# Optimization experiments

Hardware: AMD Instinct MI355X
Metric: run time of the kernel (lower is better)

## Reference

```python
import jax, jax.numpy as jnp
import numpy as np

EPS = 1e-5

def _bn(x, g, b):
    # BatchNorm1d in training mode: stats over (batch, length) dims, biased var
    mean = jnp.mean(x, axis=(0, 2), keepdims=True)
    var = jnp.var(x, axis=(0, 2), keepdims=True)
    return (x - mean) * jax.lax.rsqrt(var + EPS) * g[None, :, None] + b[None, :, None]

def _conv1x1(x, w, b):
    # pointwise Conv1d: [B,C,T] x [O,C] -> [B,O,T]
    return jnp.einsum('bct,oc->bot', x, w) + b[None, :, None]

def setup_inputs() -> dict:
    key = jax.random.key(0)
    ks = jax.random.split(key, 4)
    B, C, T = 32, 1024, 2048
    x = jax.random.normal(ks[0], (B, C, T), dtype=jnp.float32)
    w1 = jax.random.normal(ks[1], (256, 1024), dtype=jnp.float32) * (1.0 / np.sqrt(1024))
    w2 = jax.random.normal(ks[2], (64, 256), dtype=jnp.float32) * (1.0 / np.sqrt(256))
    return {
        'x': x,
        'bn1_g': jnp.ones((1024,), jnp.float32), 'bn1_b': jnp.zeros((1024,), jnp.float32),
        'w1': w1, 'b1': jnp.zeros((256,), jnp.float32),
        'bn2_g': jnp.ones((256,), jnp.float32), 'bn2_b': jnp.zeros((256,), jnp.float32),
        'w2': w2, 'b2': jnp.zeros((64,), jnp.float32),
    }

def reference(x, bn1_g, bn1_b, w1, b1, bn2_g, bn2_b, w2, b2):
    # reduction layer: BN -> 1x1 conv -> ReLU (1024 -> 256)
    h = jax.nn.relu(_conv1x1(_bn(x, bn1_g, bn1_b), w1, b1))
    # out layer: BN -> 1x1 conv, no activation (256 -> 64)
    out = _conv1x1(_bn(h, bn2_g, bn2_b), w2, b2)
    o = out.shape[1]
    mu = out[:, : o // 2, :]
    logvar = out[:, o // 2 :, :]
    return (mu, logvar)
```

## Files before the change

### kernel.cpp

```cpp
#include <hip/hip_runtime.h>

#define B_  32
#define C1  1024
#define C2  256
#define T_  2048
#define EPSF 1e-5f
#define CPAD 72

typedef __attribute__((ext_vector_type(8))) short bf16x8;
typedef __attribute__((ext_vector_type(4))) float f32x4;

static __device__ __forceinline__ unsigned short f2bf(float f) {
    union { float f; unsigned u; } v; v.f = f;
    unsigned r = v.u + 0x7fffu + ((v.u >> 16) & 1u);
    return (unsigned short)(r >> 16);
}
static __device__ __forceinline__ void g2l16(const void* g, void* l) {
    __builtin_amdgcn_global_load_lds(
        (const __attribute__((address_space(1))) unsigned int*)g,
        (__attribute__((address_space(3))) unsigned int*)l, 16, 0, 0);
}

__global__ __launch_bounds__(256) void k_prep(const float* __restrict__ x,
        unsigned short* __restrict__ xT, float* __restrict__ psum, float* __restrict__ psq) {
    __shared__ unsigned short tile[64 * CPAD];
    __shared__ float red[256];
    int ct = blockIdx.x, b = blockIdx.y, tid = threadIdx.x;
    int c0 = ct * 64;
    int cl = tid >> 2, t4 = tid & 3;
    const float* xrow = x + (size_t)b * C1 * T_ + (size_t)(c0 + cl) * T_;
    float s = 0.f, sq = 0.f;
    for (int t0 = 0; t0 < T_; t0 += 64) {
        #pragma unroll
        for (int j = 0; j < 4; ++j) {
            int tl = j * 16 + t4 * 4;
            float4 v = *(const float4*)(xrow + t0 + tl);
            s  += v.x + v.y + v.z + v.w;
            sq += v.x * v.x + v.y * v.y + v.z * v.z + v.w * v.w;
            tile[(tl + 0) * CPAD + cl] = f2bf(v.x);
            tile[(tl + 1) * CPAD + cl] = f2bf(v.y);
            tile[(tl + 2) * CPAD + cl] = f2bf(v.z);
            tile[(tl + 3) * CPAD + cl] = f2bf(v.w);
        }
        __syncthreads();
        #pragma unroll
        for (int j = 0; j < 2; ++j) {
            int w = tid + j * 256;
            int tl = w >> 3, cu = w & 7;
            uint4 vv = *(const uint4*)&tile[tl * CPAD + cu * 8];
            *(uint4*)&xT[((size_t)b * T_ + t0 + tl) * C1 + c0 + cu * 8] = vv;
        }
        __syncthreads();
    }
    red[tid] = s; __syncthreads();
    if (tid < 64)
        psum[(size_t)b * C1 + c0 + tid] = red[4*tid] + red[4*tid+1] + red[4*tid+2] + red[4*tid+3];
    __syncthreads();
    red[tid] = sq; __syncthreads();
    if (tid < 64)
        psq[(size_t)b * C1 + c0 + tid]  = red[4*tid] + red[4*tid+1] + red[4*tid+2] + red[4*tid+3];
}

__global__ __launch_bounds__(256) void k_fold1(const float* __restrict__ w1,
        const float* __restrict__ b1, const float* __restrict__ g1, const float* __restrict__ bb1,
        const float* __restrict__ psum, const float* __restrict__ psq,
        unsigned short* __restrict__ w1e, float* __restrict__ b1e) {
    int o = blockIdx.x, tid = threadIdx.x;
    int c = tid * 4;
    float4 s = {0,0,0,0}, sq = {0,0,0,0};
    for (int b = 0; b < B_; ++b) {
        float4 a = *(const float4*)(psum + (size_t)b * C1 + c);
        float4 q = *(const float4*)(psq  + (size_t)b * C1 + c);
        s.x += a.x; s.y += a.y; s.z += a.z; s.w += a.w;
        sq.x += q.x; sq.y += q.y; sq.z += q.z; sq.w += q.w;
    }
    const float n = (float)(B_ * T_);
    float4 gg = *(const float4*)(g1 + c);
    float4 bv = *(const float4*)(bb1 + c);
    float m0 = s.x / n, m1 = s.y / n, m2 = s.z / n, m3 = s.w / n;
    float sc0 = gg.x * rsqrtf(sq.x / n - m0 * m0 + EPSF);
    float sc1 = gg.y * rsqrtf(sq.y / n - m1 * m1 + EPSF);
    float sc2 = gg.z * rsqrtf(sq.z / n - m2 * m2 + EPSF);
    float sc3 = gg.w * rsqrtf(sq.w / n - m3 * m3 + EPSF);
    float sh0 = bv.x - m0 * sc0, sh1 = bv.y - m1 * sc1;
    float sh2 = bv.z - m2 * sc2, sh3 = bv.w - m3 * sc3;
    float4 w = ((const float4*)(w1 + (size_t)o * C1))[tid];
    float p = w.x * sh0 + w.y * sh1 + w.z * sh2 + w.w * sh3;
    uint2 pk;
    pk.x = (unsigned)f2bf(w.x * sc0) | ((unsigned)f2bf(w.y * sc1) << 16);
    pk.y = (unsigned)f2bf(w.z * sc2) | ((unsigned)f2bf(w.w * sc3) << 16);
    *((uint2*)(w1e + (size_t)o * C1 + c)) = pk;
    __shared__ float rs[256];
    rs[tid] = p; __syncthreads();
    for (int off = 128; off > 0; off >>= 1) {
        if (tid < off) rs[tid] += rs[tid + off];
        __syncthreads();
    }
    if (tid == 0) b1e[o] = b1[o] + rs[0];
}

__global__ __launch_bounds__(256, 2) void k_gemm1(const unsigned short* __restrict__ xT,
        const unsigned short* __restrict__ w1e, const float* __restrict__ b1e,
        unsigned short* __restrict__ hT, float* __restrict__ p2s, float* __restrict__ p2q) {
    __shared__ unsigned short sA[256 * 32];
    __shared__ unsigned short sB[128 * 32];
    int bn = blockIdx.x, b = blockIdx.y;
    int tid = threadIdx.x;
    int wave = tid >> 6, lane = tid & 63;
    int wm = wave >> 1, wn = wave & 1;
    int l15 = lane & 15, q = lane >> 4;
    f32x4 acc[8][4] = {};
    const unsigned short* xblk = xT + ((size_t)b * T_ + (size_t)bn * 128) * C1;

    for (int k0 = 0; k0 < C1; k0 += 32) {
        #pragma unroll
        for (int i = 0; i < 4; ++i) {
            int idx = (wave * 4 + i) * 64 + lane;
            int row = idx >> 2, cq = idx & 3;
            g2l16(w1e + (size_t)row * C1 + k0 + cq * 8, &sA[(wave * 4 + i) * 512]);
        }
        #pragma unroll
        for (int i = 0; i < 2; ++i) {
            int idx = (wave * 2 + i) * 64 + lane;
            int row = idx >> 2, cq = idx & 3;
            g2l16(xblk + (size_t)row * C1 + k0 + cq * 8, &sB[(wave * 2 + i) * 512]);
        }
        __syncthreads();
        bf16x8 bfr[4];
        #pragma unroll
        for (int ni = 0; ni < 4; ++ni)
            bfr[ni] = *((const bf16x8*)&sB[(wn * 64 + ni * 16 + l15) * 32 + q * 8]);
        #pragma unroll
        for (int mi = 0; mi < 8; ++mi) {
            bf16x8 af = *((const bf16x8*)&sA[(wm * 128 + mi * 16 + l15) * 32 + q * 8]);
            #pragma unroll
            for (int ni = 0; ni < 4; ++ni)
                acc[mi][ni] = __builtin_amdgcn_mfma_f32_16x16x32_bf16(af, bfr[ni], acc[mi][ni], 0, 0, 0);
        }
        __syncthreads();
    }
    int obase = wm * 128;
    int tbase = bn * 128 + wn * 64;
    int prow = (b * 16 + bn) * 2 + wn;
    #pragma unroll
    for (int mi = 0; mi < 8; ++mi) {
        int og = obase + mi * 16 + q * 4;
        float4 bias = *(const float4*)&b1e[og];
        float s0 = 0, s1 = 0, s2 = 0, s3 = 0, q0 = 0, q1 = 0, q2 = 0, q3 = 0;
        #pragma unroll
        for (int ni = 0; ni < 4; ++ni) {
            int t = tbase + ni * 16 + l15;
            float v0 = fmaxf(acc[mi][ni][0] + bias.x, 0.f);
            float v1 = fmaxf(acc[mi][ni][1] + bias.y, 0.f);
            float v2 = fmaxf(acc[mi][ni][2] + bias.z, 0.f);
            float v3 = fmaxf(acc[mi][ni][3] + bias.w, 0.f);
            s0 += v0; q0 += v0 * v0;  s1 += v1; q1 += v1 * v1;
            s2 += v2; q2 += v2 * v2;  s3 += v3; q3 += v3 * v3;
            uint2 pk;
            pk.x = (unsigned)f2bf(v0) | ((unsigned)f2bf(v1) << 16);
            pk.y = (unsigned)f2bf(v2) | ((unsigned)f2bf(v3) << 16);
            *(uint2*)&hT[((size_t)b * T_ + t) * C2 + og] = pk;
        }
        #pragma unroll
        for (int m = 1; m <= 8; m <<= 1) {
            s0 += __shfl_xor(s0, m); s1 += __shfl_xor(s1, m);
            s2 += __shfl_xor(s2, m); s3 += __shfl_xor(s3, m);
            q0 += __shfl_xor(q0, m); q1 += __shfl_xor(q1, m);
            q2 += __shfl_xor(q2, m); q3 += __shfl_xor(q3, m);
        }
        if (l15 == 0) {
            *(float4*)&p2s[(size_t)prow * C2 + og] = make_float4(s0, s1, s2, s3);
            *(float4*)&p2q[(size_t)prow * C2 + og] = make_float4(q0, q1, q2, q3);
        }
    }
}

__global__ __launch_bounds__(256) void k_fold2(const float* __restrict__ w2,
        const float* __restrict__ b2, const float* __restrict__ g2, const float* __restrict__ bb2,
        const float* __restrict__ p2s, const float* __restrict__ p2q,
        unsigned short* __restrict__ w2e, float* __restrict__ b2e) {
    int o = blockIdx.x, tid = threadIdx.x;
    float s = 0.f, sq = 0.f;
    for (int r = 0; r < 1024; ++r) {
        s  += p2s[(size_t)r * C2 + tid];
        sq += p2q[(size_t)r * C2 + tid];
    }
    const float n = (float)(B_ * T_);
    float mean = s / n;
    float sc = g2[tid] * rsqrtf(sq / n - mean * mean + EPSF);
    float sh = bb2[tid] - mean * sc;
    float w = w2[(size_t)o * C2 + tid];
    float p = w * sh;
    w2e[(size_t)o * C2 + tid] = f2bf(w * sc);
    __shared__ float rs[256];
    rs[tid] = p; __syncthreads();
    for (int off = 128; off > 0; off >>= 1) {
        if (tid < off) rs[tid] += rs[tid + off];
        __syncthreads();
    }
    if (tid == 0) b2e[o] = b2[o] + rs[0];
}

__global__ __launch_bounds__(256) void k_gemm2(const unsigned short* __restrict__ hT,
        const unsigned short* __restrict__ w2e, const float* __restrict__ b2e,
        float* __restrict__ out) {
    __shared__ unsigned short sA[64 * 32];
    __shared__ unsigned short sB[128 * 32];
    int bn = blockIdx.x, b = blockIdx.y;
    int tid = threadIdx.x;
    int wave = tid >> 6, lane = tid & 63;
    int l15 = lane & 15, q = lane >> 4;
    f32x4 acc[4][2] = {};
    const unsigned short* hblk = hT + ((size_t)b * T_ + (size_t)bn * 128) * C2;

    for (int k0 = 0; k0 < C2; k0 += 32) {
        {
            int idx = wave * 64 + lane;
            int row = idx >> 2, cq = idx & 3;
            g2l16(w2e + (size_t)row * C2 + k0 + cq * 8, &sA[wave * 512]);
        }
        #pragma unroll
        for (int i = 0; i < 2; ++i) {
            int idx = (wave * 2 + i) * 64 + lane;
            int row = idx >> 2, cq = idx & 3;
            g2l16(hblk + (size_t)row * C2 + k0 + cq * 8, &sB[(wave * 2 + i) * 512]);
        }
        __syncthreads();
        bf16x8 af[4], bfr[2];
        #pragma unroll
        for (int mi = 0; mi < 4; ++mi)
            af[mi] = *((const bf16x8*)&sA[(mi * 16 + l15) * 32 + q * 8]);
        #pragma unroll
        for (int ni = 0; ni < 2; ++ni)
            bfr[ni] = *((const bf16x8*)&sB[(wave * 32 + ni * 16 + l15) * 32 + q * 8]);
        #pragma unroll
        for (int mi = 0; mi < 4; ++mi)
            #pragma unroll
            for (int ni = 0; ni < 2; ++ni)
                acc[mi][ni] = __builtin_amdgcn_mfma_f32_16x16x32_bf16(af[mi], bfr[ni], acc[mi][ni], 0, 0, 0);
        __syncthreads();
    }
    int tbase = bn * 128 + wave * 32;
    #pragma unroll
    for (int mi = 0; mi < 4; ++mi) {
        #pragma unroll
        for (int reg = 0; reg < 4; ++reg) {
            int o = mi * 16 + q * 4 + reg;
            float bias = b2e[o];
            size_t base = (o < 32)
                ? ((size_t)b * 32 * T_ + (size_t)o * T_)
                : (2097152u + (size_t)b * 32 * T_ + (size_t)(o - 32) * T_);
            #pragma unroll
            for (int ni = 0; ni < 2; ++ni) {
                int t = tbase + ni * 16 + l15;
                out[base + t] = acc[mi][ni][reg] + bias;
            }
        }
    }
}

extern "C" void kernel_launch(void* const* d_in, const int* in_sizes, int n_in,
                              void* d_out, int out_size, void* d_ws, size_t ws_size,
                              hipStream_t stream) {
    const float* x   = (const float*)d_in[0];
    const float* g1  = (const float*)d_in[1];
    const float* bb1 = (const float*)d_in[2];
    const float* w1  = (const float*)d_in[3];
    const float* b1  = (const float*)d_in[4];
    const float* g2  = (const float*)d_in[5];
    const float* bb2 = (const float*)d_in[6];
    const float* w2  = (const float*)d_in[7];
    const float* b2  = (const float*)d_in[8];
    float* out = (float*)d_out;

    char* ws = (char*)d_ws;
    float* b1e  = (float*)(ws + 0);
    float* b2e  = (float*)(ws + 4096);
    float* psum = (float*)(ws + 8192);
    float* psq  = (float*)(ws + 139264);
    float* p2s  = (float*)(ws + 270336);
    float* p2q  = (float*)(ws + 1318912);
    unsigned short* w1e = (unsigned short*)(ws + 2367488);
    unsigned short* w2e = (unsigned short*)(ws + 2891776);
    unsigned short* xT  = (unsigned short*)(ws + 2924544);
    unsigned short* hT  = (unsigned short*)(ws + 2924544 + 134217728);

    k_prep <<<dim3(16, 32), dim3(256), 0, stream>>>(x, xT, psum, psq);
    k_fold1<<<dim3(256),    dim3(256), 0, stream>>>(w1, b1, g1, bb1, psum, psq, w1e, b1e);
    k_gemm1<<<dim3(16, 32), dim3(256), 0, stream>>>(xT, w1e, b1e, hT, p2s, p2q);
    k_fold2<<<dim3(64),     dim3(256), 0, stream>>>(w2, b2, g2, bb2, p2s, p2q, w2e, b2e);
    k_gemm2<<<dim3(16, 32), dim3(256), 0, stream>>>(hT, w2e, b2e, out);
}
```

Baseline: 536.2 us.

## Transpose x in registers without LDS and split BN1 stats into separate kernel

k_prep drops the LDS tile transpose. Each thread now loads 16 timesteps from 4 adjacent channels into registers, accumulates per-channel sum and sum of squares, and writes packed bf16 quads straight to the transposed buffer. The grid changes to 8 time-slices × 32 batches, so partial statistics grow to 256 rows. A new k_scales1 kernel reduces them once into per-channel scale and shift, which k_fold1 then reads instead of each block redoing the reduction. The aim is to remove LDS traffic and barriers, but per-thread strided row reads, a smaller grid and an extra launch may hurt memory-level parallelism.

```diff
diff --git a/kernel.cpp b/kernel.cpp
--- a/kernel.cpp
+++ b/kernel.cpp
@@ -5,7 +5,6 @@
 #define C2  256
 #define T_  2048
 #define EPSF 1e-5f
-#define CPAD 72
 
 typedef __attribute__((ext_vector_type(8))) short bf16x8;
 typedef __attribute__((ext_vector_type(4))) float f32x4;
@@ -23,72 +22,61 @@
 
 __global__ __launch_bounds__(256) void k_prep(const float* __restrict__ x,
         unsigned short* __restrict__ xT, float* __restrict__ psum, float* __restrict__ psq) {
-    __shared__ unsigned short tile[64 * CPAD];
-    __shared__ float red[256];
-    int ct = blockIdx.x, b = blockIdx.y, tid = threadIdx.x;
-    int c0 = ct * 64;
-    int cl = tid >> 2, t4 = tid & 3;
-    const float* xrow = x + (size_t)b * C1 * T_ + (size_t)(c0 + cl) * T_;
+    int tid = threadIdx.x;
+    int ts = blockIdx.x, b = blockIdx.y;
+    int c0 = tid * 4;
+    const float* xb = x + (size_t)b * C1 * T_;
+    float s0=0,s1=0,s2=0,s3=0,q0=0,q1=0,q2=0,q3=0;
+    for (int i = 0; i < 16; ++i) {
+        int t0 = ts * 256 + i * 16;
+        float a0[16], a1[16], a2[16], a3[16];
+        #pragma unroll
+        for (int j = 0; j < 4; ++j) {
+            *(float4*)&a0[j*4] = *(const float4*)(xb + (size_t)(c0+0)*T_ + t0 + j*4);
+            *(float4*)&a1[j*4] = *(const float4*)(xb + (size_t)(c0+1)*T_ + t0 + j*4);
+            *(float4*)&a2[j*4] = *(const float4*)(xb + (size_t)(c0+2)*T_ + t0 + j*4);
+            *(float4*)&a3[j*4] = *(const float4*)(xb + (size_t)(c0+3)*T_ + t0 + j*4);
+        }
+        #pragma unroll
+        for (int tt = 0; tt < 16; ++tt) {
+            float v0 = a0[tt], v1 = a1[tt], v2 = a2[tt], v3 = a3[tt];
+            s0 += v0; q0 += v0*v0;  s1 += v1; q1 += v1*v1;
+            s2 += v2; q2 += v2*v2;  s3 += v3; q3 += v3*v3;
+            uint2 pk;
+            pk.x = (unsigned)f2bf(v0) | ((unsigned)f2bf(v1) << 16);
+            pk.y = (unsigned)f2bf(v2) | ((unsigned)f2bf(v3) << 16);
+            *(uint2*)&xT[((size_t)b * T_ + t0 + tt) * C1 + c0] = pk;
+        }
+    }
+    int prow = b * 8 + ts;
+    *(float4*)&psum[(size_t)prow * C1 + c0] = make_float4(s0, s1, s2, s3);
+    *(float4*)&psq [(size_t)prow * C1 + c0] = make_float4(q0, q1, q2, q3);
+}
+
+__global__ void k_scales1(const float* __restrict__ psum, const float* __restrict__ psq,
+        const float* __restrict__ g, const float* __restrict__ bb,
+        float* __restrict__ scale, float* __restrict__ shift) {
+    int c = blockIdx.x * 256 + threadIdx.x;
     float s = 0.f, sq = 0.f;
-    for (int t0 = 0; t0 < T_; t0 += 64) {
-        #pragma unroll
-        for (int j = 0; j < 4; ++j) {
-            int tl = j * 16 + t4 * 4;
-            float4 v = *(const float4*)(xrow + t0 + tl);
-            s  += v.x + v.y + v.z + v.w;
-            sq += v.x * v.x + v.y * v.y + v.z * v.z + v.w * v.w;
-            tile[(tl + 0) * CPAD + cl] = f2bf(v.x);
-            tile[(tl + 1) * CPAD + cl] = f2bf(v.y);
-            tile[(tl + 2) * CPAD + cl] = f2bf(v.z);
-            tile[(tl + 3) * CPAD + cl] = f2bf(v.w);
-        }
-        __syncthreads();
-        #pragma unroll
-        for (int j = 0; j < 2; ++j) {
-            int w = tid + j * 256;
-            int tl = w >> 3, cu = w & 7;
-            uint4 vv = *(const uint4*)&tile[tl * CPAD + cu * 8];
-            *(uint4*)&xT[((size_t)b * T_ + t0 + tl) * C1 + c0 + cu * 8] = vv;
-        }
-        __syncthreads();
-    }
-    red[tid] = s; __syncthreads();
-    if (tid < 64)
-        psum[(size_t)b * C1 + c0 + tid] = red[4*tid] + red[4*tid+1] + red[4*tid+2] + red[4*tid+3];
-    __syncthreads();
-    red[tid] = sq; __syncthreads();
-    if (tid < 64)
-        psq[(size_t)b * C1 + c0 + tid]  = red[4*tid] + red[4*tid+1] + red[4*tid+2] + red[4*tid+3];
-}
-
-__global__ __launch_bounds__(256) void k_fold1(const float* __restrict__ w1,
-        const float* __restrict__ b1, const float* __restrict__ g1, const float* __restrict__ bb1,
-        const float* __restrict__ psum, const float* __restrict__ psq,
-        unsigned short* __restrict__ w1e, float* __restrict__ b1e) {
+    for (int r = 0; r < 256; ++r) { s += psum[(size_t)r * C1 + c]; sq += psq[(size_t)r * C1 + c]; }
+    float n = (float)(B_ * T_);
+    float mean = s / n;
+    float var  = sq / n - mean * mean;
+    float sc   = g[c] * rsqrtf(var + EPSF);
+    scale[c] = sc;
+    shift[c] = bb[c] - mean * sc;
+}
+
+__global__ void k_fold1(const float* __restrict__ w1, const float* __restrict__ b1,
+                        const float* __restrict__ scale1, const float* __restrict__ shift1,
+                        unsigned short* __restrict__ w1e, float* __restrict__ b1e) {
     int o = blockIdx.x, tid = threadIdx.x;
+    float4 w = ((const float4*)(w1 + (size_t)o * C1))[tid];
     int c = tid * 4;
-    float4 s = {0,0,0,0}, sq = {0,0,0,0};
-    for (int b = 0; b < B_; ++b) {
-        float4 a = *(const float4*)(psum + (size_t)b * C1 + c);
-        float4 q = *(const float4*)(psq  + (size_t)b * C1 + c);
-        s.x += a.x; s.y += a.y; s.z += a.z; s.w += a.w;
-        sq.x += q.x; sq.y += q.y; sq.z += q.z; sq.w += q.w;
-    }
-    const float n = (float)(B_ * T_);
-    float4 gg = *(const float4*)(g1 + c);
-    float4 bv = *(const float4*)(bb1 + c);
-    float m0 = s.x / n, m1 = s.y / n, m2 = s.z / n, m3 = s.w / n;
-    float sc0 = gg.x * rsqrtf(sq.x / n - m0 * m0 + EPSF);
-    float sc1 = gg.y * rsqrtf(sq.y / n - m1 * m1 + EPSF);
-    float sc2 = gg.z * rsqrtf(sq.z / n - m2 * m2 + EPSF);
-    float sc3 = gg.w * rsqrtf(sq.w / n - m3 * m3 + EPSF);
-    float sh0 = bv.x - m0 * sc0, sh1 = bv.y - m1 * sc1;
-    float sh2 = bv.z - m2 * sc2, sh3 = bv.w - m3 * sc3;
-    float4 w = ((const float4*)(w1 + (size_t)o * C1))[tid];
-    float p = w.x * sh0 + w.y * sh1 + w.z * sh2 + w.w * sh3;
+    float p = w.x * shift1[c] + w.y * shift1[c + 1] + w.z * shift1[c + 2] + w.w * shift1[c + 3];
     uint2 pk;
-    pk.x = (unsigned)f2bf(w.x * sc0) | ((unsigned)f2bf(w.y * sc1) << 16);
-    pk.y = (unsigned)f2bf(w.z * sc2) | ((unsigned)f2bf(w.w * sc3) << 16);
+    pk.x = (unsigned)f2bf(w.x * scale1[c])     | ((unsigned)f2bf(w.y * scale1[c + 1]) << 16);
+    pk.y = (unsigned)f2bf(w.z * scale1[c + 2]) | ((unsigned)f2bf(w.w * scale1[c + 3]) << 16);
     *((uint2*)(w1e + (size_t)o * C1 + c)) = pk;
     __shared__ float rs[256];
     rs[tid] = p; __syncthreads();
@@ -274,20 +262,23 @@
     float* out = (float*)d_out;
 
     char* ws = (char*)d_ws;
-    float* b1e  = (float*)(ws + 0);
-    float* b2e  = (float*)(ws + 4096);
-    float* psum = (float*)(ws + 8192);
-    float* psq  = (float*)(ws + 139264);
-    float* p2s  = (float*)(ws + 270336);
-    float* p2q  = (float*)(ws + 1318912);
-    unsigned short* w1e = (unsigned short*)(ws + 2367488);
-    unsigned short* w2e = (unsigned short*)(ws + 2891776);
-    unsigned short* xT  = (unsigned short*)(ws + 2924544);
-    unsigned short* hT  = (unsigned short*)(ws + 2924544 + 134217728);
-
-    k_prep <<<dim3(16, 32), dim3(256), 0, stream>>>(x, xT, psum, psq);
-    k_fold1<<<dim3(256),    dim3(256), 0, stream>>>(w1, b1, g1, bb1, psum, psq, w1e, b1e);
-    k_gemm1<<<dim3(16, 32), dim3(256), 0, stream>>>(xT, w1e, b1e, hT, p2s, p2q);
-    k_fold2<<<dim3(64),     dim3(256), 0, stream>>>(w2, b2, g2, bb2, p2s, p2q, w2e, b2e);
-    k_gemm2<<<dim3(16, 32), dim3(256), 0, stream>>>(hT, w2e, b2e, out);
-}
+    float* b1e    = (float*)(ws + 0);
+    float* b2e    = (float*)(ws + 4096);
+    float* scale1 = (float*)(ws + 8192);
+    float* shift1 = (float*)(ws + 12288);
+    float* psum   = (float*)(ws + 16384);
+    float* psq    = (float*)(ws + 1064960);
+    float* p2s    = (float*)(ws + 2113536);
+    float* p2q    = (float*)(ws + 3162112);
+    unsigned short* w1e = (unsigned short*)(ws + 4210688);
+    unsigned short* w2e = (unsigned short*)(ws + 4734976);
+    unsigned short* xT  = (unsigned short*)(ws + 4767744);
+    unsigned short* hT  = (unsigned short*)(ws + 4767744 + 134217728);
+
+    k_prep   <<<dim3(8, 32),  dim3(256), 0, stream>>>(x, xT, psum, psq);
+    k_scales1<<<dim3(4),      dim3(256), 0, stream>>>(psum, psq, g1, bb1, scale1, shift1);
+    k_fold1  <<<dim3(256),    dim3(256), 0, stream>>>(w1, b1, scale1, shift1, w1e, b1e);
+    k_gemm1  <<<dim3(16, 32), dim3(256), 0, stream>>>(xT, w1e, b1e, hT, p2s, p2q);
+    k_fold2  <<<dim3(64),     dim3(256), 0, stream>>>(w2, b2, g2, bb2, p2s, p2q, w2e, b2e);
+    k_gemm2  <<<dim3(16, 32), dim3(256), 0, stream>>>(hT, w2e, b2e, out);
+}
```

Measured after the change: 562.9 us. 1.05x slower.
